# Kernel optimization log

Hardware: AMD Instinct MI355X
Metric: run time of the kernel (lower is better)

Reference implementation:

```python
import jax, jax.numpy as jnp
import numpy as np

N, D, F, H, O, E = 100000, 128, 128, 2, 64, 400000
C = D  # per-head out channels of TransformerConv


def setup_inputs() -> dict:
    key = jax.random.key(0)
    ks = jax.random.split(key, 20)
    rn = lambda k, shape, s=0.05: (jax.random.normal(k, shape, jnp.float32) * s)
    inp = {
        "memory": rn(ks[0], (N, D), 0.1),
        # message MLP: Linear(2D+F -> D), ReLU, Linear(D -> D)
        "W1": rn(ks[1], (2 * D + F, D)), "b1": jnp.zeros((D,), jnp.float32),
        "W2": rn(ks[2], (D, D)), "b2": jnp.zeros((D,), jnp.float32),
        # GRUCell(D, D), torch layout [3D, D]
        "Wih": rn(ks[3], (3 * D, D)), "Whh": rn(ks[4], (3 * D, D)),
        "bih": jnp.zeros((3 * D,), jnp.float32), "bhh": jnp.zeros((3 * D,), jnp.float32),
        # TransformerConv projections D -> H*C (query from dst, key/value from src) + skip
        "Wq": rn(ks[5], (D, H * C)), "bq": jnp.zeros((H * C,), jnp.float32),
        "Wk": rn(ks[6], (D, H * C)), "bk": jnp.zeros((H * C,), jnp.float32),
        "Wv": rn(ks[7], (D, H * C)), "bv": jnp.zeros((H * C,), jnp.float32),
        "Ws": rn(ks[8], (D, H * C)), "bs": jnp.zeros((H * C,), jnp.float32),
        # classifier H*C -> O
        "Wc": rn(ks[9], (H * C, O)), "bc": jnp.zeros((O,), jnp.float32),
        # graph data
        "edge_attr": jax.random.normal(ks[10], (E, F), jnp.float32),
        "edge_time": jax.random.uniform(ks[11], (E,), jnp.float32),
        "edge_index": jax.random.randint(ks[12], (2, E), 0, N, jnp.int32),
    }
    return inp


def reference(memory, W1, b1, W2, b2, Wih, Whh, bih, bhh,
              Wq, bq, Wk, bk, Wv, bv, Ws, bs, Wc, bc,
              edge_attr, edge_time, edge_index):
    src, dst = edge_index[0], edge_index[1]
    src_mem = memory[src]            # [E, D] gather
    dst_mem = memory[dst]            # [E, D] gather

    # message MLP
    msg_in = jnp.concatenate([src_mem, dst_mem, edge_attr], axis=-1)  # [E, 2D+F]
    messages = jax.nn.relu(msg_in @ W1 + b1) @ W2 + b2                # [E, D]

    # GRUCell(messages, dst_mem)
    gi = messages @ Wih.T + bih
    gh = dst_mem @ Whh.T + bhh
    ir, iz, inn = jnp.split(gi, 3, axis=-1)
    hr, hz, hn = jnp.split(gh, 3, axis=-1)
    r = jax.nn.sigmoid(ir + hr)
    z = jax.nn.sigmoid(iz + hz)
    n = jnp.tanh(inn + r * hn)
    updated = (1.0 - z) * n + z * dst_mem                             # [E, D]

    x = memory.at[dst].set(updated)                                    # [N, D]

    # TransformerConv(D, D, heads=H): per-edge multi-head attention (eval: no dropout)
    q = (x @ Wq + bq).reshape(N, H, C)
    k = (x @ Wk + bk).reshape(N, H, C)
    v = (x @ Wv + bv).reshape(N, H, C)
    logits = (q[dst] * k[src]).sum(-1) / jnp.sqrt(jnp.float32(C))      # [E, H]
    m = jax.ops.segment_max(logits, dst, num_segments=N)               # [N, H]
    e = jnp.exp(logits - m[dst])
    s = jax.ops.segment_sum(e, dst, num_segments=N)                    # [N, H]
    alpha = e / s[dst]                                                 # [E, H]
    agg = jax.ops.segment_sum(alpha[:, :, None] * v[src], dst, num_segments=N)
    out = agg.reshape(N, H * C) + x @ Ws + bs                          # skip connection

    return out @ Wc + bc                                               # [N, O]
```

## Files before the change

kernel.cpp:

```cpp
#include <hip/hip_runtime.h>
#include <hip/hip_bf16.h>

#define N_NODES 100000
#define E_EDGES 400000
#define NPAD 100096

typedef unsigned short u16;
typedef __attribute__((ext_vector_type(4))) float f32x4;
typedef __attribute__((ext_vector_type(8))) short bf16x8;

__device__ inline u16 f2b(float v) {
    __hip_bfloat16 h = __float2bfloat16(v);
    return *reinterpret_cast<u16*>(&h);
}
__device__ inline float b2f(u16 u) { return __uint_as_float(((unsigned)u) << 16); }

__device__ inline void gld_lds16(const u16* g, u16* l) {
    __builtin_amdgcn_global_load_lds(
        (const __attribute__((address_space(1))) unsigned*)g,
        (__attribute__((address_space(3))) unsigned*)l, 16, 0, 0);
}

__global__ __launch_bounds__(128) void k_fold(
    const float* __restrict__ W2, const float* __restrict__ Wih,
    const float* __restrict__ Whh, const float* __restrict__ bih,
    const float* __restrict__ bhh, const float* __restrict__ b2,
    u16* __restrict__ Wcat2p, float* __restrict__ bias2) {
    int c = blockIdx.x, t = threadIdx.x;
    __shared__ float wrow[128];
    __shared__ float red[128];
    wrow[t] = (c < 384) ? Wih[c * 128 + t] : 0.f;
    __syncthreads();
    float a = 0.f;
    for (int m = 0; m < 128; ++m) a += W2[t * 128 + m] * wrow[m];
    Wcat2p[c * 256 + t] = f2b(a);
    float dv = (c < 256) ? Whh[c * 128 + t] : (c >= 384 ? Whh[(c - 128) * 128 + t] : 0.f);
    Wcat2p[c * 256 + 128 + t] = f2b(dv);
    red[t] = b2[t] * wrow[t];
    __syncthreads();
    for (int o = 64; o; o >>= 1) { if (t < o) red[t] += red[t + o]; __syncthreads(); }
    if (t == 0) {
        float b = (c < 256) ? bih[c] + bhh[c] + red[0]
                : (c < 384 ? bih[c] + red[0] : bhh[c - 128]);
        bias2[c] = b;
    }
}

__global__ __launch_bounds__(256) void k_pack(
    const float* __restrict__ W1,
    const float* __restrict__ Wq, const float* __restrict__ Wk,
    const float* __restrict__ Wv, const float* __restrict__ Ws,
    const float* __restrict__ Wc,
    const float* __restrict__ bq, const float* __restrict__ bk,
    const float* __restrict__ bv, const float* __restrict__ bs,
    const float* __restrict__ bc,
    u16* __restrict__ W1p, u16* __restrict__ Wprojp, float* __restrict__ bproj) {
    int i = blockIdx.x * 256 + threadIdx.x;
    if (i < 49152) { int n = i / 384, k2 = i % 384; W1p[i] = f2b(W1[k2 * 128 + n]); return; }
    i -= 49152;
    if (i < 98304) {
        int n = i / 128, k2 = i % 128; float v;
        if (n < 256)      v = Wq[k2 * 256 + n];
        else if (n < 512) v = Wk[k2 * 256 + (n - 256)];
        else if (n < 640) {
            int t = n - 512, h = t >> 6, o = t & 63;
            float a = 0.f;
            for (int c = 0; c < 128; ++c) a += Wv[k2 * 256 + h * 128 + c] * Wc[(h * 128 + c) * 64 + o];
            v = a;
        } else if (n < 704) {
            int o = n - 640;
            float a = 0.f;
            for (int j = 0; j < 256; ++j) a += Ws[k2 * 256 + j] * Wc[j * 64 + o];
            v = a;
        } else v = 0.f;
        Wprojp[i] = f2b(v); return;
    }
    i -= 98304;
    if (i < 768) {
        float v;
        if (i < 256)      v = bq[i];
        else if (i < 512) v = bk[i - 256];
        else if (i < 640) {
            int t = i - 512, h = t >> 6, o = t & 63;
            float a = 0.f;
            for (int c = 0; c < 128; ++c) a += bv[h * 128 + c] * Wc[(h * 128 + c) * 64 + o];
            v = a;
        } else if (i < 704) {
            int o = i - 640;
            float a = bc[o];
            for (int j = 0; j < 256; ++j) a += bs[j] * Wc[j * 64 + o];
            v = a;
        } else v = 0.f;
        bproj[i] = v;
    }
}

__global__ void k_init(int* __restrict__ winner, int* __restrict__ deg,
                       int* __restrict__ counters) {
    int n = blockIdx.x * 256 + threadIdx.x;
    if (n == 0) { counters[0] = 0; counters[1] = 0; }
    if (n < N_NODES) { winner[n] = -1; deg[n] = 0; }
}

__global__ void k_edges(const int* __restrict__ ei, int* __restrict__ winner,
                        int* __restrict__ deg) {
    int e = blockIdx.x * 256 + threadIdx.x;
    if (e < E_EDGES) {
        int dst = ei[E_EDGES + e];
        atomicMax(&winner[dst], e);
        atomicAdd(&deg[dst], 1);
    }
}

__global__ void k_nodes(const int* __restrict__ winner, const int* __restrict__ deg,
                        const int* __restrict__ ei,
                        int* __restrict__ wnode, int* __restrict__ wedge,
                        int* __restrict__ wsrc, int* __restrict__ counters,
                        int* __restrict__ startA, int* __restrict__ cursor) {
    int n = blockIdx.x * 256 + threadIdx.x;
    if (n >= N_NODES) return;
    int we = winner[n];
    if (we >= 0) {
        int i = atomicAdd(&counters[0], 1);
        wnode[i] = n;
        wedge[i] = we;
        wsrc[i] = ei[we];
    }
    int d = deg[n];
    int st = d ? atomicAdd(&counters[1], d) : 0;
    startA[n] = st;
    cursor[n] = st;
}

__global__ void k_fill(const int* __restrict__ ei, int* __restrict__ cursor,
                       int* __restrict__ esrc) {
    int e = blockIdx.x * 256 + threadIdx.x;
    if (e < E_EDGES) {
        int dst = ei[E_EDGES + e];
        int pos = atomicAdd(&cursor[dst], 1);
        esrc[pos] = ei[e];
    }
}

__global__ void k_xinit(const float* __restrict__ mem, const int* __restrict__ winner,
                        u16* __restrict__ x) {
    size_t idx = ((size_t)blockIdx.x * 256 + threadIdx.x) * 4;
    if (idx >= (size_t)N_NODES * 128) return;
    if (winner[idx >> 7] >= 0) return;
    float4 v = *(const float4*)(mem + idx);
    ushort4 o;
    o.x = f2b(v.x); o.y = f2b(v.y); o.z = f2b(v.z); o.w = f2b(v.w);
    *(ushort4*)(x + idx) = o;
}

__global__ __launch_bounds__(512, 1) void k_mg(
    const float* __restrict__ mem, const float* __restrict__ eattr,
    const int* __restrict__ wnode, const int* __restrict__ wedge,
    const int* __restrict__ wsrc, const int* __restrict__ Mp,
    const u16* __restrict__ W1p, const float* __restrict__ b1,
    const u16* __restrict__ Wcat2p, const float* __restrict__ bias2,
    u16* __restrict__ xb) {
    __shared__ u16 lB[3][128 * 64];
    __shared__ u16 h1l[2][64][136];

    const int tid = threadIdx.x;
    const int wid = tid >> 6, lane = tid & 63;
    const int grp = wid >> 2, wv = wid & 3;
    const int lrow = lane & 15, lhi = lane >> 4;
    const int M = *Mp;
    const int arow0 = blockIdx.x * 128;
    if (arow0 >= M) return;

    const int rowg = arow0 + grp * 64 + wv * 16 + lrow;
    const int rowc = min(rowg, M - 1);
    const int node = wnode[rowc];
    const int we = wedge[rowc];
    const int src = wsrc[rowc];

    bf16x8 af[12];
#pragma unroll
    for (int ks = 0; ks < 12; ++ks) {
        int c = ks * 4 + lhi;
        const float* p;
        if (c < 16)      p = mem + (size_t)src * 128 + c * 8;
        else if (c < 32) p = mem + (size_t)node * 128 + (c - 16) * 8;
        else             p = eattr + (size_t)we * 128 + (c - 32) * 8;
        float4 v0 = *(const float4*)p;
        float4 v1 = *(const float4*)(p + 4);
        bf16x8 a;
        a[0] = (short)f2b(v0.x); a[1] = (short)f2b(v0.y);
        a[2] = (short)f2b(v0.z); a[3] = (short)f2b(v0.w);
        a[4] = (short)f2b(v1.x); a[5] = (short)f2b(v1.y);
        a[6] = (short)f2b(v1.z); a[7] = (short)f2b(v1.w);
        af[ks] = a;
    }

    auto stTile = [&](int t) {
        const u16* Bp; int K, rowoff, kt;
        if (t < 6) { Bp = W1p; K = 384; rowoff = 0; kt = t; }
        else { int g = t - 6; Bp = Wcat2p; K = 256; rowoff = (g >> 2) * 128; kt = g & 3; }
        u16* dst = (u16*)lB[t % 3];
#pragma unroll
        for (int i = 0; i < 2; ++i) {
            int chunk = i * 512 + wid * 64 + lane;
            int row = chunk >> 3, cc = chunk & 7;
            int ccs = cc ^ (row & 7);
            gld_lds16(Bp + (size_t)(rowoff + row) * K + kt * 64 + ccs * 8,
                      &dst[(i * 512 + wid * 64) * 8]);
        }
    };
    stTile(0); stTile(1);

    f32x4 acc1[8] = {};
#pragma unroll
    for (int t = 0; t < 6; ++t) {
        asm volatile("s_waitcnt vmcnt(2)\ns_barrier" ::: "memory");
        __builtin_amdgcn_sched_barrier(0);
        stTile(t + 2);
        const u16* lBc = lB[t % 3];
#pragma unroll
        for (int ks = 0; ks < 2; ++ks) {
            bf16x8 bf[8];
#pragma unroll
            for (int n2 = 0; n2 < 8; ++n2) {
                int chunk = (ks * 4 + lhi) ^ (lrow & 7);
                bf[n2] = *(const bf16x8*)&lBc[(size_t)(n2 * 16 + lrow) * 64 + chunk * 8];
            }
#pragma unroll
            for (int n2 = 0; n2 < 8; ++n2)
                acc1[n2] = __builtin_amdgcn_mfma_f32_16x16x32_bf16(
                    bf[n2], af[t * 2 + ks], acc1[n2], 0, 0, 0);
        }
    }

    {
        const int rl = wv * 16 + lrow;
#pragma unroll
        for (int n2 = 0; n2 < 8; ++n2) {
            int col = n2 * 16 + lhi * 4;
            float4 bv = *(const float4*)&b1[col];
            ushort4 o;
            o.x = f2b(fmaxf(acc1[n2][0] + bv.x, 0.f));
            o.y = f2b(fmaxf(acc1[n2][1] + bv.y, 0.f));
            o.z = f2b(fmaxf(acc1[n2][2] + bv.z, 0.f));
            o.w = f2b(fmaxf(acc1[n2][3] + bv.w, 0.f));
            *(ushort4*)&h1l[grp][rl][col] = o;
        }
    }

    f32x4 accP[8] = {}, accQ[8] = {};
    bf16x8 af2[4];
#pragma unroll
    for (int tt = 0; tt < 8; ++tt) {
        if (tt == 0) {
            asm volatile("s_waitcnt vmcnt(2) lgkmcnt(0)\ns_barrier" ::: "memory");
            __builtin_amdgcn_sched_barrier(0);
        } else {
            asm volatile("s_waitcnt vmcnt(2)\ns_barrier" ::: "memory");
            __builtin_amdgcn_sched_barrier(0);
        }
        stTile(8 + tt);
        if (tt == 0) {
#pragma unroll
            for (int ks = 0; ks < 4; ++ks)
                af2[ks] = *(const bf16x8*)&h1l[grp][wv * 16 + lrow][ks * 32 + lhi * 8];
        }
        const u16* lBc = lB[(6 + tt) % 3];
#pragma unroll
        for (int ks = 0; ks < 2; ++ks) {
            const int kk = (tt & 3) * 2 + ks;
            bf16x8 a = (kk < 4) ? af2[kk] : af[kk];
            bf16x8 bf[8];
#pragma unroll
            for (int n2 = 0; n2 < 8; ++n2) {
                int chunk = (ks * 4 + lhi) ^ (lrow & 7);
                bf[n2] = *(const bf16x8*)&lBc[(size_t)(n2 * 16 + lrow) * 64 + chunk * 8];
            }
            if (tt < 4) {
#pragma unroll
                for (int n2 = 0; n2 < 8; ++n2)
                    accP[n2] = __builtin_amdgcn_mfma_f32_16x16x32_bf16(
                        bf[n2], a, accP[n2], 0, 0, 0);
            } else {
#pragma unroll
                for (int n2 = 0; n2 < 8; ++n2)
                    accQ[n2] = __builtin_amdgcn_mfma_f32_16x16x32_bf16(
                        bf[n2], a, accQ[n2], 0, 0, 0);
            }
        }
    }

    unsigned rz[32];
#pragma unroll
    for (int n2 = 0; n2 < 8; ++n2) {
        int col = n2 * 16 + lhi * 4;
        float4 br = *(const float4*)&bias2[col];
        float4 bz = *(const float4*)&bias2[128 + col];
#pragma unroll
        for (int j = 0; j < 4; ++j) {
            float bR = (j == 0) ? br.x : (j == 1) ? br.y : (j == 2) ? br.z : br.w;
            float bZ = (j == 0) ? bz.x : (j == 1) ? bz.y : (j == 2) ? bz.z : bz.w;
            float r = 1.f / (1.f + expf(-(accP[n2][j] + bR)));
            float z = 1.f / (1.f + expf(-(accQ[n2][j] + bZ)));
            rz[n2 * 4 + j] = (unsigned)f2b(r) | ((unsigned)f2b(z) << 16);
        }
        accP[n2] = (f32x4){0.f, 0.f, 0.f, 0.f};
        accQ[n2] = (f32x4){0.f, 0.f, 0.f, 0.f};
    }

#pragma unroll
    for (int tt = 0; tt < 8; ++tt) {
        if (tt <= 6) {
            asm volatile("s_waitcnt vmcnt(2)\ns_barrier" ::: "memory");
            __builtin_amdgcn_sched_barrier(0);
        } else {
            asm volatile("s_waitcnt vmcnt(0)\ns_barrier" ::: "memory");
            __builtin_amdgcn_sched_barrier(0);
        }
        if (tt <= 5) stTile(16 + tt);
        const u16* lBc = lB[(14 + tt) % 3];
#pragma unroll
        for (int ks = 0; ks < 2; ++ks) {
            const int kk = (tt & 3) * 2 + ks;
            bf16x8 a = (kk < 4) ? af2[kk] : af[kk];
            bf16x8 bf[8];
#pragma unroll
            for (int n2 = 0; n2 < 8; ++n2) {
                int chunk = (ks * 4 + lhi) ^ (lrow & 7);
                bf[n2] = *(const bf16x8*)&lBc[(size_t)(n2 * 16 + lrow) * 64 + chunk * 8];
            }
            if (tt < 4) {
#pragma unroll
                for (int n2 = 0; n2 < 8; ++n2)
                    accP[n2] = __builtin_amdgcn_mfma_f32_16x16x32_bf16(
                        bf[n2], a, accP[n2], 0, 0, 0);
            } else {
#pragma unroll
                for (int n2 = 0; n2 < 8; ++n2)
                    accQ[n2] = __builtin_amdgcn_mfma_f32_16x16x32_bf16(
                        bf[n2], a, accQ[n2], 0, 0, 0);
            }
        }
    }

    if (rowg >= M) return;
#pragma unroll
    for (int n2 = 0; n2 < 8; ++n2) {
        int col = n2 * 16 + lhi * 4;
        float4 bn = *(const float4*)&bias2[256 + col];
        float4 bh = *(const float4*)&bias2[384 + col];
        float4 hv = *(const float4*)&mem[(size_t)node * 128 + col];
        ushort4 o;
#pragma unroll
        for (int j = 0; j < 4; ++j) {
            float bN = (j == 0) ? bn.x : (j == 1) ? bn.y : (j == 2) ? bn.z : bn.w;
            float bH = (j == 0) ? bh.x : (j == 1) ? bh.y : (j == 2) ? bh.z : bh.w;
            float hj = (j == 0) ? hv.x : (j == 1) ? hv.y : (j == 2) ? hv.z : hv.w;
            unsigned p = rz[n2 * 4 + j];
            float r = b2f((u16)(p & 0xffff));
            float z = b2f((u16)(p >> 16));
            float n = tanhf(accP[n2][j] + bN + r * (accQ[n2][j] + bH));
            u16 res = f2b((1.f - z) * n + z * hj);
            if (j == 0) o.x = res; else if (j == 1) o.y = res;
            else if (j == 2) o.z = res; else o.w = res;
        }
        *(ushort4*)&xb[(size_t)node * 128 + col] = o;
    }
}

template <int K, int NQUAD>
__global__ __launch_bounds__(256, 1) void k_proj(
    const u16* __restrict__ A, const u16* __restrict__ Bp,
    const float* __restrict__ bias, int Mmax,
    u16* __restrict__ qb, u16* __restrict__ kb, u16* __restrict__ vcb,
    float* __restrict__ outf) {
    constexpr int KT = K / 64;
    constexpr int NT = NQUAD * KT;
    constexpr int NKS = K / 32;
    constexpr int CPR = K / 8;
    __shared__ u16 lA[64 * K];
    __shared__ u16 lB[3][128 * 64];

    const int tid = threadIdx.x;
    const int wid = tid >> 6, lane = tid & 63;
    const int lrow = lane & 15, lhi = lane >> 4;
    const int arow0 = blockIdx.x * 64;

#pragma unroll
    for (int i = 0; i < (64 * CPR) / 256; ++i) {
        int chunk = i * 256 + wid * 64 + lane;
        int row = chunk / CPR, cc = chunk % CPR;
        int ccs = (cc & ~7) | ((cc ^ row) & 7);
        gld_lds16(A + (size_t)(arow0 + row) * K + ccs * 8, &lA[(i * 256 + wid * 64) * 8]);
    }
    auto stTile = [&](int t) {
        int q = t / KT, kt = t - q * KT;
        u16* dst = (u16*)lB[t % 3];
#pragma unroll
        for (int i = 0; i < 4; ++i) {
            int chunk = i * 256 + wid * 64 + lane;
            int row = chunk >> 3, cc = chunk & 7;
            int ccs = cc ^ (row & 7);
            gld_lds16(Bp + (size_t)(q * 128 + row) * K + kt * 64 + ccs * 8,
                      &dst[(i * 256 + wid * 64) * 8]);
        }
    };
    stTile(0); stTile(1);
    asm volatile("s_waitcnt vmcnt(8)\ns_barrier" ::: "memory");
    __builtin_amdgcn_sched_barrier(0);

    bf16x8 af[NKS];
#pragma unroll
    for (int ks = 0; ks < NKS; ++ks) {
        int chunk = ks * 4 + lhi;
        int ccs = (chunk & ~7) | ((chunk ^ lrow) & 7);
        af[ks] = *(const bf16x8*)&lA[(size_t)(wid * 16 + lrow) * K + ccs * 8];
    }

    f32x4 acc[NQUAD][8] = {};
#pragma unroll
    for (int t = 0; t < NT; ++t) {
        if (t <= NT - 2) {
            asm volatile("s_waitcnt vmcnt(4)\ns_barrier" ::: "memory");
            __builtin_amdgcn_sched_barrier(0);
        } else {
            asm volatile("s_waitcnt vmcnt(0)\ns_barrier" ::: "memory");
            __builtin_amdgcn_sched_barrier(0);
        }
        if (t + 2 < NT) stTile(t + 2);
        const int q = t / KT, kt = t - q * KT;
        const u16* lBc = lB[t % 3];
#pragma unroll
        for (int ks = 0; ks < 2; ++ks) {
            bf16x8 bf[8];
#pragma unroll
            for (int n2 = 0; n2 < 8; ++n2) {
                int chunk = (ks * 4 + lhi) ^ (lrow & 7);
                bf[n2] = *(const bf16x8*)&lBc[(size_t)(n2 * 16 + lrow) * 64 + chunk * 8];
            }
#pragma unroll
            for (int n2 = 0; n2 < 8; ++n2)
                acc[q][n2] = __builtin_amdgcn_mfma_f32_16x16x32_bf16(
                    bf[n2], af[kt * 2 + ks], acc[q][n2], 0, 0, 0);
        }
    }

    const int rowg = arow0 + wid * 16 + lrow;
    if (rowg >= Mmax) return;

#pragma unroll
    for (int q = 0; q < NQUAD; ++q) {
#pragma unroll
        for (int n2 = 0; n2 < 8; ++n2) {
            int colg = q * 128 + n2 * 16 + lhi * 4;
            if (colg >= 704) continue;
            float4 bv = *(const float4*)&bias[colg];
            float v0 = acc[q][n2][0] + bv.x, v1 = acc[q][n2][1] + bv.y;
            float v2 = acc[q][n2][2] + bv.z, v3 = acc[q][n2][3] + bv.w;
            if (colg < 640) {
                ushort4 o;
                o.x = f2b(v0); o.y = f2b(v1); o.z = f2b(v2); o.w = f2b(v3);
                if (colg < 256)
                    *(ushort4*)&qb[(size_t)rowg * 256 + colg] = o;
                else if (colg < 512)
                    *(ushort4*)&kb[(size_t)rowg * 256 + (colg - 256)] = o;
                else
                    *(ushort4*)&vcb[(size_t)rowg * 128 + (colg - 512)] = o;
            } else {
                float4 o; o.x = v0; o.y = v1; o.z = v2; o.w = v3;
                *(float4*)&outf[(size_t)rowg * 64 + (colg - 640)] = o;
            }
        }
    }
}

__global__ __launch_bounds__(256) void k_attn(
    const u16* __restrict__ qB, const u16* __restrict__ kB, const u16* __restrict__ vcB,
    const int* __restrict__ startA, const int* __restrict__ deg,
    const int* __restrict__ esrc, float* __restrict__ out) {
    int wid = threadIdx.x >> 6, lane = threadIdx.x & 63;
    int dst = blockIdx.x * 4 + wid;
    if (dst >= N_NODES) return;
    int d = deg[dst];
    if (d == 0) return;
    int st = startA[dst];

    ushort4 qv = *(const ushort4*)&qB[(size_t)dst * 256 + lane * 4];
    float q0 = b2f(qv.x), q1 = b2f(qv.y), q2 = b2f(qv.z), q3 = b2f(qv.w);
    const float inv = 0.08838834764831845f;

    float s0 = 0.f, s1 = 0.f, accA = 0.f, accB = 0.f;
    int src = esrc[st];
    for (int p = st; p < st + d; ++p) {
        int src_next = (p + 1 < st + d) ? esrc[p + 1] : 0;
        ushort4 kv = *(const ushort4*)&kB[(size_t)src * 256 + lane * 4];
        float v0 = b2f(vcB[(size_t)src * 128 + lane]);
        float v1 = b2f(vcB[(size_t)src * 128 + 64 + lane]);
        float pp = q0 * b2f(kv.x) + q1 * b2f(kv.y) + q2 * b2f(kv.z) + q3 * b2f(kv.w);
        pp += __shfl_xor(pp, 1);
        pp += __shfl_xor(pp, 2);
        pp += __shfl_xor(pp, 4);
        pp += __shfl_xor(pp, 8);
        pp += __shfl_xor(pp, 16);
        float e = expf(pp * inv);
        float eo = __shfl_xor(e, 32);
        float e0 = (lane < 32) ? e : eo;
        float e1 = (lane < 32) ? eo : e;
        s0 += e0; s1 += e1;
        accA += e0 * v0;
        accB += e1 * v1;
        src = src_next;
    }
    float* op = out + (size_t)dst * 64 + lane;
    *op += accA / s0 + accB / s1;
}

extern "C" void kernel_launch(void* const* d_in, const int* in_sizes, int n_in,
                              void* d_out, int out_size, void* d_ws, size_t ws_size,
                              hipStream_t stream) {
    const float* memory = (const float*)d_in[0];
    const float* W1 = (const float*)d_in[1];  const float* b1 = (const float*)d_in[2];
    const float* W2 = (const float*)d_in[3];  const float* b2 = (const float*)d_in[4];
    const float* Wih = (const float*)d_in[5]; const float* Whh = (const float*)d_in[6];
    const float* bih = (const float*)d_in[7]; const float* bhh = (const float*)d_in[8];
    const float* Wq = (const float*)d_in[9];  const float* bq = (const float*)d_in[10];
    const float* Wk = (const float*)d_in[11]; const float* bk = (const float*)d_in[12];
    const float* Wv = (const float*)d_in[13]; const float* bv = (const float*)d_in[14];
    const float* Ws = (const float*)d_in[15]; const float* bs = (const float*)d_in[16];
    const float* Wc = (const float*)d_in[17]; const float* bc = (const float*)d_in[18];
    const float* eattr = (const float*)d_in[19];
    const int* ei = (const int*)d_in[21];
    float* out = (float*)d_out;

    char* ws = (char*)d_ws;
    size_t off = 0;
    auto alloc = [&](size_t bytes) -> char* {
        char* p = ws + off;
        off = (off + bytes + 255) & ~(size_t)255;
        return p;
    };
    u16* xb = (u16*)alloc((size_t)NPAD * 128 * 2);
    u16* qb = (u16*)alloc((size_t)NPAD * 256 * 2);
    u16* kb = (u16*)alloc((size_t)NPAD * 256 * 2);
    u16* vcb = (u16*)alloc((size_t)NPAD * 128 * 2);
    int* winner = (int*)alloc((size_t)N_NODES * 4);
    int* wnode = (int*)alloc((size_t)N_NODES * 4);
    int* wedge = (int*)alloc((size_t)N_NODES * 4);
    int* wsrc = (int*)alloc((size_t)N_NODES * 4);
    int* deg = (int*)alloc((size_t)N_NODES * 4);
    int* startA = (int*)alloc((size_t)N_NODES * 4);
    int* cursor = (int*)alloc((size_t)N_NODES * 4);
    int* esrc = (int*)alloc((size_t)E_EDGES * 4);
    int* counters = (int*)alloc(256);
    u16* W1p = (u16*)alloc(49152 * 2);
    u16* Wcat2p = (u16*)alloc(131072 * 2);
    u16* Wprojp = (u16*)alloc(98304 * 2);
    float* bias2 = (float*)alloc(512 * 4);
    float* bproj = (float*)alloc(768 * 4);
    (void)ws_size; (void)in_sizes; (void)n_in; (void)out_size;

    int* wcount = counters;

    hipLaunchKernelGGL(k_init, dim3(391), dim3(256), 0, stream, winner, deg, counters);
    hipLaunchKernelGGL(k_edges, dim3(1563), dim3(256), 0, stream, ei, winner, deg);
    hipLaunchKernelGGL(k_nodes, dim3(391), dim3(256), 0, stream,
                       winner, deg, ei, wnode, wedge, wsrc, counters, startA, cursor);
    hipLaunchKernelGGL(k_fill, dim3(1563), dim3(256), 0, stream, ei, cursor, esrc);
    hipLaunchKernelGGL(k_pack, dim3(579), dim3(256), 0, stream,
                       W1, Wq, Wk, Wv, Ws, Wc, bq, bk, bv, bs, bc, W1p, Wprojp, bproj);
    hipLaunchKernelGGL(k_fold, dim3(512), dim3(128), 0, stream,
                       W2, Wih, Whh, bih, bhh, b2, Wcat2p, bias2);
    hipLaunchKernelGGL(k_xinit, dim3(12500), dim3(256), 0, stream, memory, winner, xb);
    hipLaunchKernelGGL(k_mg, dim3(782), dim3(512), 0, stream,
                       memory, eattr, wnode, wedge, wsrc, wcount,
                       W1p, b1, Wcat2p, bias2, xb);
    hipLaunchKernelGGL((k_proj<128, 6>), dim3(1564), dim3(256), 0, stream,
                       xb, Wprojp, bproj, N_NODES, qb, kb, vcb, out);
    hipLaunchKernelGGL(k_attn, dim3(25000), dim3(256), 0, stream,
                       qb, kb, vcb, startA, deg, esrc, out);
}
```

Baseline: 387.2 us.

## Share projection weight tiles across two row groups and split accumulators into halves

```diff
diff --git a/kernel.cpp b/kernel.cpp
--- a/kernel.cpp
+++ b/kernel.cpp
@@ -368,95 +368,62 @@
     }
 }
 
-template <int K, int NQUAD>
-__global__ __launch_bounds__(256, 1) void k_proj(
+__global__ __launch_bounds__(512, 1) void k_proj(
     const u16* __restrict__ A, const u16* __restrict__ Bp,
     const float* __restrict__ bias, int Mmax,
     u16* __restrict__ qb, u16* __restrict__ kb, u16* __restrict__ vcb,
     float* __restrict__ outf) {
-    constexpr int KT = K / 64;
-    constexpr int NT = NQUAD * KT;
-    constexpr int NKS = K / 32;
-    constexpr int CPR = K / 8;
-    __shared__ u16 lA[64 * K];
+    __shared__ u16 lA[2][64 * 128];
     __shared__ u16 lB[3][128 * 64];
 
     const int tid = threadIdx.x;
     const int wid = tid >> 6, lane = tid & 63;
+    const int grp = wid >> 2, wv = wid & 3;
     const int lrow = lane & 15, lhi = lane >> 4;
-    const int arow0 = blockIdx.x * 64;
-
-#pragma unroll
-    for (int i = 0; i < (64 * CPR) / 256; ++i) {
-        int chunk = i * 256 + wid * 64 + lane;
-        int row = chunk / CPR, cc = chunk % CPR;
+    const int arow0 = blockIdx.x * 128;
+
+#pragma unroll
+    for (int i = 0; i < 4; ++i) {
+        int chunk = i * 256 + wv * 64 + lane;
+        int row = chunk >> 4, cc = chunk & 15;
         int ccs = (cc & ~7) | ((cc ^ row) & 7);
-        gld_lds16(A + (size_t)(arow0 + row) * K + ccs * 8, &lA[(i * 256 + wid * 64) * 8]);
+        gld_lds16(A + (size_t)(arow0 + grp * 64 + row) * 128 + ccs * 8,
+                  &lA[grp][(i * 256 + wv * 64) * 8]);
     }
     auto stTile = [&](int t) {
-        int q = t / KT, kt = t - q * KT;
+        int q = t >> 1, kt = t & 1;
         u16* dst = (u16*)lB[t % 3];
 #pragma unroll
-        for (int i = 0; i < 4; ++i) {
-            int chunk = i * 256 + wid * 64 + lane;
+        for (int i = 0; i < 2; ++i) {
+            int chunk = i * 512 + wid * 64 + lane;
             int row = chunk >> 3, cc = chunk & 7;
             int ccs = cc ^ (row & 7);
-            gld_lds16(Bp + (size_t)(q * 128 + row) * K + kt * 64 + ccs * 8,
-                      &dst[(i * 256 + wid * 64) * 8]);
+            gld_lds16(Bp + (size_t)(q * 128 + row) * 128 + kt * 64 + ccs * 8,
+                      &dst[(i * 512 + wid * 64) * 8]);
         }
     };
     stTile(0); stTile(1);
-    asm volatile("s_waitcnt vmcnt(8)\ns_barrier" ::: "memory");
+    asm volatile("s_waitcnt vmcnt(4)\ns_barrier" ::: "memory");
     __builtin_amdgcn_sched_barrier(0);
 
-    bf16x8 af[NKS];
-#pragma unroll
-    for (int ks = 0; ks < NKS; ++ks) {
+    bf16x8 af[4];
+#pragma unroll
+    for (int ks = 0; ks < 4; ++ks) {
         int chunk = ks * 4 + lhi;
         int ccs = (chunk & ~7) | ((chunk ^ lrow) & 7);
-        af[ks] = *(const bf16x8*)&lA[(size_t)(wid * 16 + lrow) * K + ccs * 8];
-    }
-
-    f32x4 acc[NQUAD][8] = {};
-#pragma unroll
-    for (int t = 0; t < NT; ++t) {
-        if (t <= NT - 2) {
-            asm volatile("s_waitcnt vmcnt(4)\ns_barrier" ::: "memory");
-            __builtin_amdgcn_sched_barrier(0);
-        } else {
-            asm volatile("s_waitcnt vmcnt(0)\ns_barrier" ::: "memory");
-            __builtin_amdgcn_sched_barrier(0);
-        }
-        if (t + 2 < NT) stTile(t + 2);
-        const int q = t / KT, kt = t - q * KT;
-        const u16* lBc = lB[t % 3];
-#pragma unroll
-        for (int ks = 0; ks < 2; ++ks) {
-            bf16x8 bf[8];
-#pragma unroll
-            for (int n2 = 0; n2 < 8; ++n2) {
-                int chunk = (ks * 4 + lhi) ^ (lrow & 7);
-                bf[n2] = *(const bf16x8*)&lBc[(size_t)(n2 * 16 + lrow) * 64 + chunk * 8];
-            }
-#pragma unroll
-            for (int n2 = 0; n2 < 8; ++n2)
-                acc[q][n2] = __builtin_amdgcn_mfma_f32_16x16x32_bf16(
-                    bf[n2], af[kt * 2 + ks], acc[q][n2], 0, 0, 0);
-        }
-    }
-
-    const int rowg = arow0 + wid * 16 + lrow;
-    if (rowg >= Mmax) return;
-
-#pragma unroll
-    for (int q = 0; q < NQUAD; ++q) {
+        af[ks] = *(const bf16x8*)&lA[grp][(size_t)(wv * 16 + lrow) * 128 + ccs * 8];
+    }
+
+    const int rowg = arow0 + grp * 64 + wv * 16 + lrow;
+    auto storeq = [&](int q, f32x4 (&aq)[8]) {
+        if (rowg >= Mmax) return;
 #pragma unroll
         for (int n2 = 0; n2 < 8; ++n2) {
             int colg = q * 128 + n2 * 16 + lhi * 4;
             if (colg >= 704) continue;
             float4 bv = *(const float4*)&bias[colg];
-            float v0 = acc[q][n2][0] + bv.x, v1 = acc[q][n2][1] + bv.y;
-            float v2 = acc[q][n2][2] + bv.z, v3 = acc[q][n2][3] + bv.w;
+            float v0 = aq[n2][0] + bv.x, v1 = aq[n2][1] + bv.y;
+            float v2 = aq[n2][2] + bv.z, v3 = aq[n2][3] + bv.w;
             if (colg < 640) {
                 ushort4 o;
                 o.x = f2b(v0); o.y = f2b(v1); o.z = f2b(v2); o.w = f2b(v3);
@@ -471,7 +438,90 @@
                 *(float4*)&outf[(size_t)rowg * 64 + (colg - 640)] = o;
             }
         }
-    }
+    };
+
+    f32x4 accA[8] = {}, accB[8] = {}, accC[8] = {};
+#pragma unroll
+    for (int t = 0; t < 6; ++t) {
+        asm volatile("s_waitcnt vmcnt(2)\ns_barrier" ::: "memory");
+        __builtin_amdgcn_sched_barrier(0);
+        stTile(t + 2);
+        const int qi = t >> 1;
+        const u16* lBc = lB[t % 3];
+#pragma unroll
+        for (int ks = 0; ks < 2; ++ks) {
+            bf16x8 bf[8];
+#pragma unroll
+            for (int n2 = 0; n2 < 8; ++n2) {
+                int chunk = (ks * 4 + lhi) ^ (lrow & 7);
+                bf[n2] = *(const bf16x8*)&lBc[(size_t)(n2 * 16 + lrow) * 64 + chunk * 8];
+            }
+            if (qi == 0) {
+#pragma unroll
+                for (int n2 = 0; n2 < 8; ++n2)
+                    accA[n2] = __builtin_amdgcn_mfma_f32_16x16x32_bf16(
+                        bf[n2], af[(t & 1) * 2 + ks], accA[n2], 0, 0, 0);
+            } else if (qi == 1) {
+#pragma unroll
+                for (int n2 = 0; n2 < 8; ++n2)
+                    accB[n2] = __builtin_amdgcn_mfma_f32_16x16x32_bf16(
+                        bf[n2], af[(t & 1) * 2 + ks], accB[n2], 0, 0, 0);
+            } else {
+#pragma unroll
+                for (int n2 = 0; n2 < 8; ++n2)
+                    accC[n2] = __builtin_amdgcn_mfma_f32_16x16x32_bf16(
+                        bf[n2], af[(t & 1) * 2 + ks], accC[n2], 0, 0, 0);
+            }
+        }
+    }
+    storeq(0, accA); storeq(1, accB); storeq(2, accC);
+#pragma unroll
+    for (int n2 = 0; n2 < 8; ++n2) {
+        accA[n2] = (f32x4){0.f, 0.f, 0.f, 0.f};
+        accB[n2] = (f32x4){0.f, 0.f, 0.f, 0.f};
+        accC[n2] = (f32x4){0.f, 0.f, 0.f, 0.f};
+    }
+
+#pragma unroll
+    for (int tt = 0; tt < 6; ++tt) {
+        if (tt <= 4) {
+            asm volatile("s_waitcnt vmcnt(2)\ns_barrier" ::: "memory");
+            __builtin_amdgcn_sched_barrier(0);
+        } else {
+            asm volatile("s_waitcnt vmcnt(0)\ns_barrier" ::: "memory");
+            __builtin_amdgcn_sched_barrier(0);
+        }
+        if (tt <= 3) stTile(8 + tt);
+        const int t = 6 + tt;
+        const int qi = tt >> 1;
+        const u16* lBc = lB[t % 3];
+#pragma unroll
+        for (int ks = 0; ks < 2; ++ks) {
+            bf16x8 bf[8];
+#pragma unroll
+            for (int n2 = 0; n2 < 8; ++n2) {
+                int chunk = (ks * 4 + lhi) ^ (lrow & 7);
+                bf[n2] = *(const bf16x8*)&lBc[(size_t)(n2 * 16 + lrow) * 64 + chunk * 8];
+            }
+            if (qi == 0) {
+#pragma unroll
+                for (int n2 = 0; n2 < 8; ++n2)
+                    accA[n2] = __builtin_amdgcn_mfma_f32_16x16x32_bf16(
+                        bf[n2], af[(tt & 1) * 2 + ks], accA[n2], 0, 0, 0);
+            } else if (qi == 1) {
+#pragma unroll
+                for (int n2 = 0; n2 < 8; ++n2)
+                    accB[n2] = __builtin_amdgcn_mfma_f32_16x16x32_bf16(
+                        bf[n2], af[(tt & 1) * 2 + ks], accB[n2], 0, 0, 0);
+            } else {
+#pragma unroll
+                for (int n2 = 0; n2 < 8; ++n2)
+                    accC[n2] = __builtin_amdgcn_mfma_f32_16x16x32_bf16(
+                        bf[n2], af[(tt & 1) * 2 + ks], accC[n2], 0, 0, 0);
+            }
+        }
+    }
+    storeq(3, accA); storeq(4, accB); storeq(5, accC);
 }
 
 __global__ __launch_bounds__(256) void k_attn(
@@ -574,7 +624,7 @@
     hipLaunchKernelGGL(k_mg, dim3(782), dim3(512), 0, stream,
                        memory, eattr, wnode, wedge, wsrc, wcount,
                        W1p, b1, Wcat2p, bias2, xb);
-    hipLaunchKernelGGL((k_proj<128, 6>), dim3(1564), dim3(256), 0, stream,
+    hipLaunchKernelGGL(k_proj, dim3(782), dim3(512), 0, stream,
                        xb, Wprojp, bproj, N_NODES, qb, kb, vcb, out);
     hipLaunchKernelGGL(k_attn, dim3(25000), dim3(256), 0, stream,
                        qb, kb, vcb, startA, deg, esrc, out);
```

New measurement: 381.4 us. No clear change (-1.5%).
